# Kernel tuning notes

Measured on AMD Instinct MI355X. Metric: run time of the kernel, lower is better.

The kernel has to match this reference:

```python
import jax, jax.numpy as jnp
import numpy as np

N_NODES = 50000
N_EDGES = 800000
HID = 64
N_LAYERS = 3
N_GRAPHS = 64
NEG_SLOPE = 0.01  # nn.LeakyReLU default


def setup_inputs() -> dict:
    key = jax.random.key(0)
    ks = jax.random.split(key, 10)
    return {
        "x": jax.random.normal(ks[0], (N_NODES, HID), dtype=jnp.float32),
        "edge_attr": jax.random.normal(ks[1], (N_EDGES,), dtype=jnp.float32),
        "edge_w": jax.random.normal(ks[2], (N_LAYERS, 1, HID), dtype=jnp.float32) * 0.1,
        "edge_b": jax.random.normal(ks[3], (N_LAYERS, HID), dtype=jnp.float32) * 0.1,
        "node_w": jax.random.normal(ks[4], (N_LAYERS, 2 * HID, HID), dtype=jnp.float32) * 0.05,
        "node_b": jax.random.normal(ks[5], (N_LAYERS, HID), dtype=jnp.float32) * 0.1,
        "fc_w": jax.random.normal(ks[6], (HID, 1), dtype=jnp.float32) * 0.1,
        "fc_b": jax.random.normal(ks[7], (1,), dtype=jnp.float32) * 0.1,
        "edge_index": jax.random.randint(ks[8], (2, N_EDGES), 0, N_NODES, dtype=jnp.int32),
        "batch": jnp.sort(jax.random.randint(ks[9], (N_NODES,), 0, N_GRAPHS, dtype=jnp.int32)),
    }


def reference(x, edge_attr, edge_w, edge_b, node_w, node_b, fc_w, fc_b, edge_index, batch):
    src = edge_index[0]  # x_j gathered from source nodes
    dst = edge_index[1]  # aggregated into target nodes (aggr='add')
    ea = edge_attr.reshape(-1, 1)  # [E, 1]
    for l in range(N_LAYERS):
        edge_emb = ea @ edge_w[l] + edge_b[l]                       # [E, H] edge MLP
        msg = jnp.concatenate([x[src], edge_emb], axis=1)            # [E, 2H] message
        aggr = jax.ops.segment_sum(msg, dst, num_segments=N_NODES)   # [N, 2H] scatter-add
        x = jax.nn.relu(aggr @ node_w[l] + node_b[l])                # update: node MLP + ReLU
        x = jnp.where(x >= 0, x, NEG_SLOPE * x)                      # LeakyReLU (dropout=0)
    # global_mean_pool over batch assignment
    sums = jax.ops.segment_sum(x, batch, num_segments=N_GRAPHS)      # [G, H]
    counts = jax.ops.segment_sum(jnp.ones((x.shape[0], 1), x.dtype), batch, num_segments=N_GRAPHS)
    pooled = sums / jnp.maximum(counts, 1.0)
    return pooled @ fc_w + fc_b  # [G, 1]
```

## Files before the change

kernel.cpp:

```cpp
#include <hip/hip_runtime.h>

#define N_NODES 50000
#define N_EDGES 800000
#define HID 64
#define N_LAYERS 3
#define N_GRAPHS 64
#define MAXDEG 64
#define FIXS 4096.0f

typedef unsigned int u32;
typedef unsigned short ushort_t;
typedef short bf16x8 __attribute__((ext_vector_type(8)));
typedef float f32x4 __attribute__((ext_vector_type(4)));

__device__ __forceinline__ ushort_t f2bf(float f) {
    unsigned int u = __builtin_bit_cast(unsigned int, f);
    unsigned int r = u + 0x7fffu + ((u >> 16) & 1u);
    return (ushort_t)(r >> 16);
}
__device__ __forceinline__ float lo16(u32 u) { return __builtin_bit_cast(float, u << 16); }
__device__ __forceinline__ float hi16(u32 u) { return __builtin_bit_cast(float, u & 0xffff0000u); }

__global__ __launch_bounds__(256) void edge_cvt_uv_kernel(
        const int* __restrict__ src, const int* __restrict__ dst,
        const float* __restrict__ ea,
        int* __restrict__ cnt, u32* __restrict__ ell,
        const float* __restrict__ x_in, uint4* __restrict__ xbf0,
        const int* __restrict__ batch, int* __restrict__ gstart,
        const float* __restrict__ edge_w, const float* __restrict__ edge_b,
        const float* __restrict__ node_w, float* __restrict__ uv,
        int edgeBlocks, int cvtBlocks, int gbBlocks) {
    int t = threadIdx.x;
    int b = (int)blockIdx.x;
    if (b < edgeBlocks) {
        int e = b * 256 + t;
        if (e >= N_EDGES) return;
        int d = dst[e];
        float fv = (ea[e] + 8.0f) * FIXS;
        fv = fminf(fmaxf(fv, 0.0f), 65535.0f);
        u32 fx = __float2uint_rn(fv);
        int pos = atomicAdd(&cnt[d], 1);
        if (pos < MAXDEG) ell[((size_t)d << 6) + pos] = (u32)src[e] | (fx << 16);
        return;
    }
    if (b < edgeBlocks + cvtBlocks) {
        int i = (b - edgeBlocks) * 256 + t;
        if (i < N_NODES * HID / 8) {
            const float4* p = (const float4*)(x_in + (size_t)i * 8);
            float4 a = p[0], c = p[1];
            uint4 o;
            o.x = (u32)f2bf(a.x) | ((u32)f2bf(a.y) << 16);
            o.y = (u32)f2bf(a.z) | ((u32)f2bf(a.w) << 16);
            o.z = (u32)f2bf(c.x) | ((u32)f2bf(c.y) << 16);
            o.w = (u32)f2bf(c.z) | ((u32)f2bf(c.w) << 16);
            xbf0[i] = o;
        }
        return;
    }
    if (b < edgeBlocks + cvtBlocks + gbBlocks) {
        int i = (b - edgeBlocks - cvtBlocks) * 256 + t;
        if (i >= N_NODES) return;
        int bi = batch[i];
        if (i == 0) {
            for (int g = 0; g <= bi; g++) gstart[g] = 0;
        } else {
            int bp = batch[i - 1];
            for (int g = bp + 1; g <= bi; g++) gstart[g] = i;
        }
        if (i == N_NODES - 1) {
            for (int g = bi + 1; g <= N_GRAPHS; g++) gstart[g] = N_NODES;
        }
        return;
    }
    if (t >= N_LAYERS * HID) return;
    int l = t >> 6, hp = t & 63;
    const float* w2 = node_w + l * 2 * HID * HID + HID * HID + hp;
    float u = 0.f, v = 0.f;
    for (int h = 0; h < HID; h++) {
        float w = w2[h * HID];
        u += edge_w[l * HID + h] * w;
        v += edge_b[l * HID + h] * w;
    }
    uv[l * 2 * HID + hp]       = u;
    uv[l * 2 * HID + HID + hp] = v;
}

__global__ __launch_bounds__(128) void agg_mfma_kernel(
        const ushort_t* __restrict__ xbf, const u32* __restrict__ ell,
        const int* __restrict__ cnt,
        const float* __restrict__ W1, const float* __restrict__ node_b_l,
        const float* __restrict__ uv_l, float* __restrict__ sattr,
        int layer0, ushort_t* __restrict__ out_bf, float* __restrict__ out_f32) {
    __shared__ float redA[64][9];
    __shared__ float redB[64][9];
    __shared__ u32   redS[64];
    int lane = threadIdx.x & 63;
    int half = threadIdx.x >> 6;
    int nodeBase = blockIdx.x * 16;
    int q = lane >> 4, n15 = lane & 15;

    int m = nodeBase + n15;
    int dg = cnt[m]; if (dg > MAXDEG) dg = MAXDEG;
    int mx = dg;
#pragma unroll
    for (int off = 1; off < 16; off <<= 1) {
        int o = __shfl_xor(mx, off);
        mx = o > mx ? o : mx;
    }

    const uint4* erow4 = (const uint4*)(ell + ((size_t)m << 6));
    const uint4* xrows = (const uint4*)xbf;
    float accA[8] = {0,0,0,0,0,0,0,0};
    float accB[8] = {0,0,0,0,0,0,0,0};
    u32 sfix = 0;
    int base = half * 4;
    uint4 e4 = {0, 0, 0, 0};
    if (base < mx) e4 = erow4[base >> 2];
    for (; base < mx; base += 8) {
        int nbase = base + 8;
        uint4 e4n = {0, 0, 0, 0};
        if (nbase < mx) e4n = erow4[nbase >> 2];
        u32 ee[4] = {e4.x, e4.y, e4.z, e4.w};
        uint4 lo[4], hi[4];
        float f[4];
#pragma unroll
        for (int k = 0; k < 4; k++) {
            bool v = (base + k) < dg;
            u32 e = ee[k];
            sfix += v ? (e >> 16) : 0u;
            int s = v ? (int)(e & 0xffffu) : 0;
            lo[k] = xrows[(size_t)s * 8 + q];
            hi[k] = xrows[(size_t)s * 8 + 4 + q];
            f[k] = v ? 1.0f : 0.0f;
        }
#pragma unroll
        for (int k = 0; k < 4; k++) {
            accA[0] += f[k] * lo16(lo[k].x); accA[1] += f[k] * hi16(lo[k].x);
            accA[2] += f[k] * lo16(lo[k].y); accA[3] += f[k] * hi16(lo[k].y);
            accA[4] += f[k] * lo16(lo[k].z); accA[5] += f[k] * hi16(lo[k].z);
            accA[6] += f[k] * lo16(lo[k].w); accA[7] += f[k] * hi16(lo[k].w);
            accB[0] += f[k] * lo16(hi[k].x); accB[1] += f[k] * hi16(hi[k].x);
            accB[2] += f[k] * lo16(hi[k].y); accB[3] += f[k] * hi16(hi[k].y);
            accB[4] += f[k] * lo16(hi[k].z); accB[5] += f[k] * hi16(hi[k].z);
            accB[6] += f[k] * lo16(hi[k].w); accB[7] += f[k] * hi16(hi[k].w);
        }
        e4 = e4n;
    }

    if (half == 1) {
#pragma unroll
        for (int j = 0; j < 8; j++) { redA[lane][j] = accA[j]; redB[lane][j] = accB[j]; }
        redS[lane] = sfix;
    }
    __syncthreads();
    if (half == 1) return;
#pragma unroll
    for (int j = 0; j < 8; j++) { accA[j] += redA[lane][j]; accB[j] += redB[lane][j]; }
    sfix += redS[lane];

    float satv;
    if (layer0) {
        satv = (float)(int)sfix * (1.0f / FIXS) - 8.0f * (float)dg;
        if (lane < 16) sattr[nodeBase + lane] = satv;
    } else {
        satv = sattr[m];
    }

    bf16x8 af0, af1;
#pragma unroll
    for (int j = 0; j < 8; j++) {
        af0[j] = (short)f2bf(accA[j]);
        af1[j] = (short)f2bf(accB[j]);
    }

    int q8 = q * 8;
    f32x4 c[4];
#pragma unroll
    for (int nt = 0; nt < 4; nt++) {
        bf16x8 b0, b1;
#pragma unroll
        for (int j = 0; j < 8; j++) {
            b0[j] = (short)f2bf(W1[(q8 + j) * HID + nt * 16 + n15]);
            b1[j] = (short)f2bf(W1[(32 + q8 + j) * HID + nt * 16 + n15]);
        }
        f32x4 z = {0.f, 0.f, 0.f, 0.f};
        c[nt] = __builtin_amdgcn_mfma_f32_16x16x32_bf16(af0, b0, z, 0, 0, 0);
        c[nt] = __builtin_amdgcn_mfma_f32_16x16x32_bf16(af1, b1, c[nt], 0, 0, 0);
    }

    float dgown = (float)dg;
    float sat[4], dgf[4];
#pragma unroll
    for (int r = 0; r < 4; r++) {
        int srcLane = q * 4 + r;
        sat[r] = __shfl(satv, srcLane);
        dgf[r] = __shfl(dgown, srcLane);
    }
#pragma unroll
    for (int nt = 0; nt < 4; nt++) {
        int col = nt * 16 + n15;
        float uc = uv_l[col], vc = uv_l[HID + col], bc = node_b_l[col];
#pragma unroll
        for (int r = 0; r < 4; r++) {
            int n = nodeBase + q * 4 + r;
            float val = c[nt][r] + sat[r] * uc + dgf[r] * vc + bc;
            val = val > 0.f ? val : 0.f;
            if (out_bf) out_bf[(size_t)n * HID + col] = f2bf(val);
            else        out_f32[(size_t)n * HID + col] = val;
        }
    }
}

__global__ __launch_bounds__(256) void pool_fc_kernel(
        const float* __restrict__ x, const int* __restrict__ gstart,
        const float* __restrict__ fc_w, const float* __restrict__ fc_b,
        float* __restrict__ out) {
    __shared__ float red[4][HID];
    int g = blockIdx.x;
    int lane = threadIdx.x & 63, w = threadIdx.x >> 6;
    int s = gstart[g], e = gstart[g + 1];
    float acc = 0.f;
    int r = s + w;
    for (; r + 12 < e; r += 16) {
        float a0 = x[(size_t)(r     ) * HID + lane];
        float a1 = x[(size_t)(r +  4) * HID + lane];
        float a2 = x[(size_t)(r +  8) * HID + lane];
        float a3 = x[(size_t)(r + 12) * HID + lane];
        acc += a0 + a1 + a2 + a3;
    }
    for (; r < e; r += 4) acc += x[(size_t)r * HID + lane];
    red[w][lane] = acc;
    __syncthreads();
    if (w != 0) return;
    acc = red[0][lane] + red[1][lane] + red[2][lane] + red[3][lane];
    float dot = acc * fc_w[lane];
    for (int off = 32; off > 0; off >>= 1) dot += __shfl_down(dot, off);
    if (lane == 0) {
        float cntf = (float)(e - s);
        if (cntf < 1.f) cntf = 1.f;
        out[g] = dot / cntf + fc_b[0];
    }
}

extern "C" void kernel_launch(void* const* d_in, const int* in_sizes, int n_in,
                              void* d_out, int out_size, void* d_ws, size_t ws_size,
                              hipStream_t stream) {
    const float* x_in      = (const float*)d_in[0];
    const float* edge_attr = (const float*)d_in[1];
    const float* edge_w    = (const float*)d_in[2];
    const float* edge_b    = (const float*)d_in[3];
    const float* node_w    = (const float*)d_in[4];
    const float* node_b    = (const float*)d_in[5];
    const float* fc_w      = (const float*)d_in[6];
    const float* fc_b      = (const float*)d_in[7];
    const int*   edge_index= (const int*)d_in[8];
    const int*   batch     = (const int*)d_in[9];
    float* out = (float*)d_out;

    ushort_t* xbf0  = (ushort_t*)d_ws;
    ushort_t* xbf1  = xbf0 + (size_t)N_NODES * HID;
    float*    xA    = (float*)(xbf1 + (size_t)N_NODES * HID);
    u32*      ell   = (u32*)(xA + (size_t)N_NODES * HID);
    int*      cnt   = (int*)(ell + (size_t)N_NODES * MAXDEG);
    int*      gstart= cnt + N_NODES;
    float*    sattr = (float*)(gstart + N_GRAPHS + 1);
    float*    uv    = sattr + N_NODES;

    const int* src = edge_index;
    const int* dst = edge_index + N_EDGES;

    hipMemsetAsync(cnt, 0, (size_t)N_NODES * sizeof(int), stream);

    const int EB  = (N_EDGES + 255) / 256;
    const int CVT = (N_NODES * HID / 8 + 255) / 256;
    const int GB  = (N_NODES + 255) / 256;
    edge_cvt_uv_kernel<<<EB + CVT + GB + 1, 256, 0, stream>>>(
        src, dst, edge_attr, cnt, ell, x_in, (uint4*)xbf0, batch, gstart,
        edge_w, edge_b, node_w, uv, EB, CVT, GB);

    const int AGG_BLOCKS = N_NODES / 16;
    agg_mfma_kernel<<<AGG_BLOCKS, 128, 0, stream>>>(
        xbf0, ell, cnt, node_w, node_b, uv, sattr, 1, xbf1, nullptr);
    agg_mfma_kernel<<<AGG_BLOCKS, 128, 0, stream>>>(
        xbf1, ell, cnt, node_w + (size_t)2 * HID * HID, node_b + HID, uv + 2 * HID,
        sattr, 0, xbf0, nullptr);
    agg_mfma_kernel<<<AGG_BLOCKS, 128, 0, stream>>>(
        xbf0, ell, cnt, node_w + (size_t)4 * HID * HID, node_b + 2 * HID, uv + 4 * HID,
        sattr, 0, nullptr, xA);

    pool_fc_kernel<<<N_GRAPHS, 256, 0, stream>>>(xA, gstart, fc_w, fc_b, out);
}
```

Baseline: 215.9 us.

## Split bf16 node features into low/high half arrays and gather in two passes

Stores the bf16 node feature matrix as two separate arrays, columns 0-31 and columns 32-63, each 64 bytes per node. The aggregation kernel now gathers all neighbours' low halves in one loop and the high halves in a second loop over the same edge list. The aim is to shrink the working set each pass touches so the random gathers hit cache more often. The cost is reading the ELL edge row twice, and each pass has fewer loads in flight per iteration.

```diff
diff --git a/kernel.cpp b/kernel.cpp
--- a/kernel.cpp
+++ b/kernel.cpp
@@ -25,11 +25,11 @@
         const int* __restrict__ src, const int* __restrict__ dst,
         const float* __restrict__ ea,
         int* __restrict__ cnt, u32* __restrict__ ell,
-        const float* __restrict__ x_in, uint4* __restrict__ xbf0,
+        const float* __restrict__ x_in, uint4* __restrict__ xlo0, uint4* __restrict__ xhi0,
         const int* __restrict__ batch, int* __restrict__ gstart,
         const float* __restrict__ edge_w, const float* __restrict__ edge_b,
         const float* __restrict__ node_w, float* __restrict__ uv,
-        int edgeBlocks, int cvtBlocks, int gbBlocks) {
+        int edgeBlocks, int cvtBlocks) {
     int t = threadIdx.x;
     int b = (int)blockIdx.x;
     if (b < edgeBlocks) {
@@ -46,18 +46,20 @@
     if (b < edgeBlocks + cvtBlocks) {
         int i = (b - edgeBlocks) * 256 + t;
         if (i < N_NODES * HID / 8) {
-            const float4* p = (const float4*)(x_in + (size_t)i * 8);
+            int n = i >> 3, j = i & 7;
+            const float4* p = (const float4*)(x_in + (size_t)n * HID + j * 8);
             float4 a = p[0], c = p[1];
             uint4 o;
             o.x = (u32)f2bf(a.x) | ((u32)f2bf(a.y) << 16);
             o.y = (u32)f2bf(a.z) | ((u32)f2bf(a.w) << 16);
             o.z = (u32)f2bf(c.x) | ((u32)f2bf(c.y) << 16);
             o.w = (u32)f2bf(c.z) | ((u32)f2bf(c.w) << 16);
-            xbf0[i] = o;
+            if (j < 4) xlo0[(size_t)n * 4 + j]       = o;
+            else       xhi0[(size_t)n * 4 + (j - 4)] = o;
         }
         return;
     }
-    if (b < edgeBlocks + cvtBlocks + gbBlocks) {
+    if (b < edgeBlocks + cvtBlocks + ((N_NODES + 255) / 256)) {
         int i = (b - edgeBlocks - cvtBlocks) * 256 + t;
         if (i >= N_NODES) return;
         int bi = batch[i];
@@ -86,11 +88,12 @@
 }
 
 __global__ __launch_bounds__(128) void agg_mfma_kernel(
-        const ushort_t* __restrict__ xbf, const u32* __restrict__ ell,
-        const int* __restrict__ cnt,
+        const ushort_t* __restrict__ xlo, const ushort_t* __restrict__ xhi,
+        const u32* __restrict__ ell, const int* __restrict__ cnt,
         const float* __restrict__ W1, const float* __restrict__ node_b_l,
         const float* __restrict__ uv_l, float* __restrict__ sattr,
-        int layer0, ushort_t* __restrict__ out_bf, float* __restrict__ out_f32) {
+        int layer0, ushort_t* __restrict__ olo, ushort_t* __restrict__ ohi,
+        float* __restrict__ out_f32) {
     __shared__ float redA[64][9];
     __shared__ float redB[64][9];
     __shared__ u32   redS[64];
@@ -109,42 +112,67 @@
     }
 
     const uint4* erow4 = (const uint4*)(ell + ((size_t)m << 6));
-    const uint4* xrows = (const uint4*)xbf;
+    const uint4* plo = (const uint4*)xlo;
+    const uint4* phi = (const uint4*)xhi;
     float accA[8] = {0,0,0,0,0,0,0,0};
     float accB[8] = {0,0,0,0,0,0,0,0};
     u32 sfix = 0;
-    int base = half * 4;
-    uint4 e4 = {0, 0, 0, 0};
-    if (base < mx) e4 = erow4[base >> 2];
-    for (; base < mx; base += 8) {
-        int nbase = base + 8;
-        uint4 e4n = {0, 0, 0, 0};
-        if (nbase < mx) e4n = erow4[nbase >> 2];
-        u32 ee[4] = {e4.x, e4.y, e4.z, e4.w};
-        uint4 lo[4], hi[4];
-        float f[4];
-#pragma unroll
-        for (int k = 0; k < 4; k++) {
-            bool v = (base + k) < dg;
-            u32 e = ee[k];
-            sfix += v ? (e >> 16) : 0u;
-            int s = v ? (int)(e & 0xffffu) : 0;
-            lo[k] = xrows[(size_t)s * 8 + q];
-            hi[k] = xrows[(size_t)s * 8 + 4 + q];
-            f[k] = v ? 1.0f : 0.0f;
-        }
-#pragma unroll
-        for (int k = 0; k < 4; k++) {
-            accA[0] += f[k] * lo16(lo[k].x); accA[1] += f[k] * hi16(lo[k].x);
-            accA[2] += f[k] * lo16(lo[k].y); accA[3] += f[k] * hi16(lo[k].y);
-            accA[4] += f[k] * lo16(lo[k].z); accA[5] += f[k] * hi16(lo[k].z);
-            accA[6] += f[k] * lo16(lo[k].w); accA[7] += f[k] * hi16(lo[k].w);
-            accB[0] += f[k] * lo16(hi[k].x); accB[1] += f[k] * hi16(hi[k].x);
-            accB[2] += f[k] * lo16(hi[k].y); accB[3] += f[k] * hi16(hi[k].y);
-            accB[4] += f[k] * lo16(hi[k].z); accB[5] += f[k] * hi16(hi[k].z);
-            accB[6] += f[k] * lo16(hi[k].w); accB[7] += f[k] * hi16(hi[k].w);
-        }
-        e4 = e4n;
+
+    {
+        int base = half * 4;
+        uint4 e4 = {0,0,0,0};
+        if (base < mx) e4 = erow4[base >> 2];
+        for (; base < mx; base += 8) {
+            int nbase = base + 8;
+            uint4 e4n = {0,0,0,0};
+            if (nbase < mx) e4n = erow4[nbase >> 2];
+            u32 ee[4] = {e4.x, e4.y, e4.z, e4.w};
+            uint4 r[4]; float f[4];
+#pragma unroll
+            for (int k = 0; k < 4; k++) {
+                bool v = (base + k) < dg;
+                u32 e = ee[k];
+                sfix += v ? (e >> 16) : 0u;
+                int s = v ? (int)(e & 0xffffu) : 0;
+                r[k] = plo[(size_t)s * 4 + q];
+                f[k] = v ? 1.0f : 0.0f;
+            }
+#pragma unroll
+            for (int k = 0; k < 4; k++) {
+                accA[0] += f[k] * lo16(r[k].x); accA[1] += f[k] * hi16(r[k].x);
+                accA[2] += f[k] * lo16(r[k].y); accA[3] += f[k] * hi16(r[k].y);
+                accA[4] += f[k] * lo16(r[k].z); accA[5] += f[k] * hi16(r[k].z);
+                accA[6] += f[k] * lo16(r[k].w); accA[7] += f[k] * hi16(r[k].w);
+            }
+            e4 = e4n;
+        }
+    }
+    {
+        int base = half * 4;
+        uint4 e4 = {0,0,0,0};
+        if (base < mx) e4 = erow4[base >> 2];
+        for (; base < mx; base += 8) {
+            int nbase = base + 8;
+            uint4 e4n = {0,0,0,0};
+            if (nbase < mx) e4n = erow4[nbase >> 2];
+            u32 ee[4] = {e4.x, e4.y, e4.z, e4.w};
+            uint4 r[4]; float f[4];
+#pragma unroll
+            for (int k = 0; k < 4; k++) {
+                bool v = (base + k) < dg;
+                int s = v ? (int)(ee[k] & 0xffffu) : 0;
+                r[k] = phi[(size_t)s * 4 + q];
+                f[k] = v ? 1.0f : 0.0f;
+            }
+#pragma unroll
+            for (int k = 0; k < 4; k++) {
+                accB[0] += f[k] * lo16(r[k].x); accB[1] += f[k] * hi16(r[k].x);
+                accB[2] += f[k] * lo16(r[k].y); accB[3] += f[k] * hi16(r[k].y);
+                accB[4] += f[k] * lo16(r[k].z); accB[5] += f[k] * hi16(r[k].z);
+                accB[6] += f[k] * lo16(r[k].w); accB[7] += f[k] * hi16(r[k].w);
+            }
+            e4 = e4n;
+        }
     }
 
     if (half == 1) {
@@ -205,8 +233,9 @@
             int n = nodeBase + q * 4 + r;
             float val = c[nt][r] + sat[r] * uc + dgf[r] * vc + bc;
             val = val > 0.f ? val : 0.f;
-            if (out_bf) out_bf[(size_t)n * HID + col] = f2bf(val);
-            else        out_f32[(size_t)n * HID + col] = val;
+            if (out_f32) out_f32[(size_t)n * HID + col] = val;
+            else if (nt < 2) olo[(size_t)n * 32 + col]        = f2bf(val);
+            else             ohi[(size_t)n * 32 + (col - 32)] = f2bf(val);
         }
     }
 }
@@ -257,9 +286,11 @@
     const int*   batch     = (const int*)d_in[9];
     float* out = (float*)d_out;
 
-    ushort_t* xbf0  = (ushort_t*)d_ws;
-    ushort_t* xbf1  = xbf0 + (size_t)N_NODES * HID;
-    float*    xA    = (float*)(xbf1 + (size_t)N_NODES * HID);
+    ushort_t* xloA  = (ushort_t*)d_ws;
+    ushort_t* xhiA  = xloA + (size_t)N_NODES * 32;
+    ushort_t* xloB  = xhiA + (size_t)N_NODES * 32;
+    ushort_t* xhiB  = xloB + (size_t)N_NODES * 32;
+    float*    xA    = (float*)(xhiB + (size_t)N_NODES * 32);
     u32*      ell   = (u32*)(xA + (size_t)N_NODES * HID);
     int*      cnt   = (int*)(ell + (size_t)N_NODES * MAXDEG);
     int*      gstart= cnt + N_NODES;
@@ -275,18 +306,18 @@
     const int CVT = (N_NODES * HID / 8 + 255) / 256;
     const int GB  = (N_NODES + 255) / 256;
     edge_cvt_uv_kernel<<<EB + CVT + GB + 1, 256, 0, stream>>>(
-        src, dst, edge_attr, cnt, ell, x_in, (uint4*)xbf0, batch, gstart,
-        edge_w, edge_b, node_w, uv, EB, CVT, GB);
+        src, dst, edge_attr, cnt, ell, x_in, (uint4*)xloA, (uint4*)xhiA, batch, gstart,
+        edge_w, edge_b, node_w, uv, EB, CVT);
 
     const int AGG_BLOCKS = N_NODES / 16;
     agg_mfma_kernel<<<AGG_BLOCKS, 128, 0, stream>>>(
-        xbf0, ell, cnt, node_w, node_b, uv, sattr, 1, xbf1, nullptr);
+        xloA, xhiA, ell, cnt, node_w, node_b, uv, sattr, 1, xloB, xhiB, nullptr);
     agg_mfma_kernel<<<AGG_BLOCKS, 128, 0, stream>>>(
-        xbf1, ell, cnt, node_w + (size_t)2 * HID * HID, node_b + HID, uv + 2 * HID,
-        sattr, 0, xbf0, nullptr);
+        xloB, xhiB, ell, cnt, node_w + (size_t)2 * HID * HID, node_b + HID, uv + 2 * HID,
+        sattr, 0, xloA, xhiA, nullptr);
     agg_mfma_kernel<<<AGG_BLOCKS, 128, 0, stream>>>(
-        xbf0, ell, cnt, node_w + (size_t)4 * HID * HID, node_b + 2 * HID, uv + 4 * HID,
-        sattr, 0, nullptr, xA);
+        xloA, xhiA, ell, cnt, node_w + (size_t)4 * HID * HID, node_b + 2 * HID, uv + 4 * HID,
+        sattr, 0, nullptr, nullptr, xA);
 
     pool_fc_kernel<<<N_GRAPHS, 256, 0, stream>>>(xA, gstart, fc_w, fc_b, out);
 }
```

New measurement: 217.2 us. No clear change (+0.6%).
